# Kernel tuning notes

Hardware: AMD Instinct MI355X
Metric: run time of the kernel (lower is better)

## Reference

```python
import jax, jax.numpy as jnp
import numpy as np


def setup_inputs() -> dict:
    key = jax.random.key(0)
    k1, k2, k3 = jax.random.split(key, 3)
    B, T, J, D = 32, 1024, 128, 256  # D = 2 * input_dim
    ctx_embd = jax.random.normal(k1, (B, T, D), dtype=jnp.float32)
    query_embd = jax.random.normal(k2, (B, J, D), dtype=jnp.float32)
    # nn.Linear(6*input_dim, 1, bias=False) weight flattened: [w1 | w2 | w3], each of size D
    w = jax.random.normal(k3, (3 * D,), dtype=jnp.float32) * (1.0 / np.sqrt(3 * D))
    return {"ctx_embd": ctx_embd, "query_embd": query_embd, "w": w}


def reference(ctx_embd, query_embd, w):
    D = ctx_embd.shape[-1]
    w1, w2, w3 = w[:D], w[D:2 * D], w[2 * D:]
    # Trilinear score S[b,t,j] = ctx.w1 + query.w2 + (ctx*query).w3, decomposed
    # (algebraically identical to Linear(cat(ctx, query, ctx*query))).
    s_ctx = ctx_embd @ w1            # [B, T]
    s_qry = query_embd @ w2          # [B, J]
    s_mul = jnp.einsum('btd,bjd->btj', ctx_embd * w3, query_embd)  # [B, T, J]
    S = s_ctx[:, :, None] + s_qry[:, None, :] + s_mul              # [B, T, J]
    # Context-to-query attention
    a = jax.nn.softmax(S, axis=-1)                                 # [B, T, J]
    c2q = jnp.einsum('btj,bjd->btd', a, query_embd)                # [B, T, D]
    # Query-to-context attention
    b = jax.nn.softmax(jnp.max(S, axis=2), axis=-1)                # [B, T]
    q2c = jnp.einsum('bt,btd->bd', b, ctx_embd)[:, None, :]        # [B, 1, D] broadcast over T
    G = jnp.concatenate(
        [ctx_embd, c2q, ctx_embd * c2q, ctx_embd * q2c], axis=-1)  # [B, T, 4D]
    return G
```

## Files before the change

### kernel.cpp

```cpp
#include <hip/hip_runtime.h>

typedef float f4 __attribute__((ext_vector_type(4)));
typedef float f2 __attribute__((ext_vector_type(2)));
typedef short s8v __attribute__((ext_vector_type(8)));
typedef unsigned int u2v __attribute__((ext_vector_type(2)));
typedef unsigned int u4v __attribute__((ext_vector_type(4)));

#define B_ 32
#define T_ 1024
#define J_ 128
#define D_ 256

__device__ inline unsigned short f2bf(float x) {
    unsigned int u = __float_as_uint(x);
    u += 0x7fffu + ((u >> 16) & 1u);
    return (unsigned short)(u >> 16);
}

__device__ __forceinline__ void ldsload16(const void* g, void* l) {
    __builtin_amdgcn_global_load_lds(
        (const __attribute__((address_space(1))) void*)g,
        (__attribute__((address_space(3))) void*)l, 16, 0, 0);
}

__global__ __launch_bounds__(256) void k_pre(const float* __restrict__ q, const float* __restrict__ w,
                                             unsigned short* __restrict__ Bqh, float* __restrict__ sq,
                                             unsigned short* __restrict__ qTh) {
    __shared__ float t_[16][260];
    int b = blockIdx.x >> 3, jt = blockIdx.x & 7;
    int tid = threadIdx.x;
    const float* qb = q + (b * J_ + jt * 16) * D_;

#pragma unroll
    for (int k = 0; k < 4; k++) {
        int idx = tid + (k << 8);
        int jj = idx >> 6, d4 = idx & 63;
        f4 v = *(const f4*)(qb + jj * D_ + (d4 << 2));
        *(f4*)&t_[jj][d4 << 2] = v;
        f4 w1v = *(const f4*)(w + (d4 << 2));
        f4 w3v = *(const f4*)(w + 2 * D_ + (d4 << 2));
        u2v p;
        p[0] = (unsigned int)f2bf(w3v[0] * v[0] + w1v[0]) | ((unsigned int)f2bf(w3v[1] * v[1] + w1v[1]) << 16);
        p[1] = (unsigned int)f2bf(w3v[2] * v[2] + w1v[2]) | ((unsigned int)f2bf(w3v[3] * v[3] + w1v[3]) << 16);
        *(u2v*)(Bqh + (b * J_ + jt * 16 + jj) * D_ + (d4 << 2)) = p;
    }
    __syncthreads();

    {
        int jj = tid >> 4, dg = tid & 15;
        float p = 0.f;
#pragma unroll
        for (int i = 0; i < 16; i++) {
            int d = (dg << 4) + i;
            p += t_[jj][d] * w[D_ + d];
        }
#pragma unroll
        for (int m = 8; m >= 1; m >>= 1) p += __shfl_xor(p, m);
        if (dg == 0) sq[b * J_ + jt * 16 + jj] = p;
    }

    {
        int dd = tid;
        unsigned int pk[8];
#pragma unroll
        for (int i = 0; i < 8; i++) {
            pk[i] = (unsigned int)f2bf(t_[2 * i][dd]) | ((unsigned int)f2bf(t_[2 * i + 1][dd]) << 16);
        }
        u4v v0, v1;
        v0[0] = pk[0]; v0[1] = pk[1]; v0[2] = pk[2]; v0[3] = pk[3];
        v1[0] = pk[4]; v1[1] = pk[5]; v1[2] = pk[6]; v1[3] = pk[7];
        unsigned short* dst = qTh + (b * D_ + dd) * J_ + jt * 16;
        *(u4v*)dst = v0;
        *(u4v*)(dst + 8) = v1;
    }
}

__global__ __launch_bounds__(256, 4) void k_main(const float* __restrict__ ctx,
                                                 const unsigned short* __restrict__ Bqh,
                                                 const unsigned short* __restrict__ qTh,
                                                 const float* __restrict__ sq,
                                                 float* __restrict__ pq2c, float* __restrict__ pms,
                                                 float* __restrict__ out) {
    __shared__ __align__(16) char lds[40960];
    char* B0 = lds;
    char* B1 = lds + 16384;
    char* Ps = lds + 32768;
    float* sc = (float*)B1;

    int bid = blockIdx.x;
    int b  = ((bid & 7) << 2) | ((bid >> 3) & 3);
    int tc = bid >> 5;
    int t0 = tc << 5;
    int tid = threadIdx.x;
    int w = tid >> 6, l = tid & 63, lr = l & 15, lq = l >> 4;
    int rg = w & 1, ch = w >> 1;
    int R0 = rg << 4;

    const unsigned short* BqB  = Bqh + b * J_ * D_;
    const unsigned short* qThB = qTh + b * D_ * J_;

    auto stageBq = [&](char* buf, int qt) {
#pragma unroll
        for (int i = 0; i < 4; i++) {
            int g = tid + (i << 8);
            int jr = g >> 3, c = g & 7;
            ldsload16(BqB + jr * D_ + (qt << 6) + ((c ^ (jr & 7)) << 3),
                      buf + (i << 12) + (w << 10));
        }
    };
    auto stageQ = [&](char* buf, int st) {
#pragma unroll
        for (int i = 0; i < 4; i++) {
            int g = tid + (i << 8);
            int dr = g >> 4, c = g & 15;
            ldsload16(qThB + ((st << 6) + dr) * J_ + ((c ^ (dr & 7)) << 3),
                      buf + (i << 12) + (w << 10));
        }
    };

    f4 acc[4];
#pragma unroll
    for (int nf = 0; nf < 4; nf++) acc[nf] = (f4){0.f, 0.f, 0.f, 0.f};

    stageBq(B0, 0);
    stageBq(B1, 1);

    const float* ctxA = ctx + (b * T_ + t0 + R0 + lr) * D_;
    s8v af[8];
#pragma unroll
    for (int k = 0; k < 8; k++) {
        f4 a0 = *(const f4*)(ctxA + k * 32 + lq * 8);
        f4 a1 = *(const f4*)(ctxA + k * 32 + lq * 8 + 4);
        union { unsigned short u[8]; s8v v; } t;
#pragma unroll
        for (int e = 0; e < 4; e++) { t.u[e] = f2bf(a0[e]); t.u[e + 4] = f2bf(a1[e]); }
        af[k] = t.v;
    }

    auto mfmaA = [&](char* buf, int qt) {
#pragma unroll
        for (int kk = 0; kk < 2; kk++)
#pragma unroll
            for (int nf = 0; nf < 4; nf++) {
                int jr = (ch << 6) + (nf << 4) + lr;
                s8v bv = *(const s8v*)(buf + (jr << 7) + ((((kk << 2) | lq) ^ (jr & 7)) << 4));
                acc[nf] = __builtin_amdgcn_mfma_f32_16x16x32_bf16(af[(qt << 1) | kk], bv, acc[nf], 0, 0, 0);
            }
    };

    __syncthreads();
    mfmaA(B0, 0);
    __syncthreads();
    stageBq(B0, 2);
    mfmaA(B1, 1);
    __syncthreads();
    stageBq(B1, 3);
    mfmaA(B0, 2);
    __syncthreads();
    stageQ(B0, 0);
    mfmaA(B1, 3);

    float sqv[4];
#pragma unroll
    for (int nf = 0; nf < 4; nf++) sqv[nf] = sq[b * J_ + (ch << 6) + (nf << 4) + lr];
    float mp[4], sp[4];
#pragma unroll
    for (int r = 0; r < 4; r++) {
        float m = -1e30f;
#pragma unroll
        for (int nf = 0; nf < 4; nf++) { acc[nf][r] += sqv[nf]; m = fmaxf(m, acc[nf][r]); }
#pragma unroll
        for (int msk = 8; msk >= 1; msk >>= 1) m = fmaxf(m, __shfl_xor(m, msk));
        float s = 0.f;
#pragma unroll
        for (int nf = 0; nf < 4; nf++) { float e = __expf(acc[nf][r] - m); acc[nf][r] = e; s += e; }
#pragma unroll
        for (int msk = 8; msk >= 1; msk >>= 1) s += __shfl_xor(s, msk);
        mp[r] = m; sp[r] = s;
    }
    __syncthreads();
    if (lr == 0) {
#pragma unroll
        for (int r = 0; r < 4; r++) {
            int row = R0 + (lq << 2) + r;
            sc[(row << 2) + (ch << 1)] = mp[r];
            sc[(row << 2) + (ch << 1) + 1] = sp[r];
        }
    }
    __syncthreads();

    float mm[4];
#pragma unroll
    for (int r = 0; r < 4; r++) {
        int row = R0 + (lq << 2) + r;
        float m0 = sc[(row << 2)],     s0 = sc[(row << 2) + 1];
        float m1 = sc[(row << 2) + 2], s1 = sc[(row << 2) + 3];
        float m = fmaxf(m0, m1);
        float sum = s0 * __expf(m0 - m) + s1 * __expf(m1 - m);
        float scale = __expf(mp[r] - m) / sum;
#pragma unroll
        for (int nf = 0; nf < 4; nf++) {
            int cc = (ch << 6) + (nf << 4) + lr;
            int chunk = cc >> 3;
            *(unsigned short*)(Ps + row * 256 + ((chunk ^ (row & 7)) << 4) + ((lr & 7) << 1)) =
                f2bf(acc[nf][r] * scale);
        }
        mm[r] = m;
    }
    __syncthreads();
    stageQ(B1, 1);

    int prow = R0 + lr;
    s8v pf[4];
#pragma unroll
    for (int jk = 0; jk < 4; jk++)
        pf[jk] = *(const s8v*)(Ps + prow * 256 + ((((jk << 2) + lq) ^ (prow & 7)) << 4));

    f4 acc2[8];
#pragma unroll
    for (int ai = 0; ai < 8; ai++) acc2[ai] = (f4){0.f, 0.f, 0.f, 0.f};

    auto mfmaB = [&](char* rb, int s) {
#pragma unroll
        for (int df2 = 0; df2 < 2; df2++) {
            int dr = (ch << 5) + (df2 << 4) + lr;
            int ai = (s << 1) + df2;
#pragma unroll
            for (int jk = 0; jk < 4; jk++) {
                s8v bv = *(const s8v*)(rb + (dr << 8) + ((((jk << 2) + lq) ^ (dr & 7)) << 4));
                acc2[ai] = __builtin_amdgcn_mfma_f32_16x16x32_bf16(pf[jk], bv, acc2[ai], 0, 0, 0);
            }
        }
    };

    mfmaB(B0, 0);
    __syncthreads();
    stageQ(B0, 2);
    mfmaB(B1, 1);
    __syncthreads();
    stageQ(B1, 3);
    mfmaB(B0, 2);
    __syncthreads();
    mfmaB(B1, 3);
    __syncthreads();

    float* cq = (float*)lds;
#pragma unroll
    for (int s2 = 0; s2 < 4; s2++)
#pragma unroll
        for (int df2 = 0; df2 < 2; df2++) {
            int col = (s2 << 6) + (ch << 5) + (df2 << 4) + lr;
            int ai = (s2 << 1) + df2;
            int chunk = col >> 2;
#pragma unroll
            for (int r = 0; r < 4; r++) {
                int row = R0 + (lq << 2) + r;
                *(float*)((char*)cq + (row << 10) + ((chunk ^ (row & 7)) << 4) + ((col & 3) << 2)) = acc2[ai][r];
            }
        }
    __syncthreads();

    {
        int row = tid >> 3;
        int o = b * T_ + t0 + row;
        const float* crow = ctx + o * D_;
        float* orow = out + o * 1024;
#pragma unroll
        for (int i = 0; i < 8; i++) {
            int col4 = (i << 5) + ((tid & 7) << 2);
            int chunk = col4 >> 2;
            f4 val = *(const f4*)((char*)cq + (row << 10) + ((chunk ^ (row & 7)) << 4));
            f4 cx = *(const f4*)(crow + col4);
            f4 v3 = cx * val;
            __builtin_nontemporal_store(cx, (f4*)(orow + col4));
            __builtin_nontemporal_store(val, (f4*)(orow + 256 + col4));
            __builtin_nontemporal_store(v3, (f4*)(orow + 512 + col4));
        }
    }

    {
        float m16[16];
#pragma unroll
        for (int i = 0; i < 16; i++) m16[i] = __shfl(mm[i & 3], (i >> 2) << 4);
        float mw = -1e30f;
#pragma unroll
        for (int i = 0; i < 16; i++) mw = fmaxf(mw, m16[i]);
        const float* cp = ctx + (b * T_ + t0 + R0) * D_ + (ch << 7) + (l << 1);
        f2 p = (f2){0.f, 0.f};
        float sw_ = 0.f;
#pragma unroll 4
        for (int t = 0; t < 16; t++) {
            float e = __expf(m16[t] - mw);
            sw_ += e;
            f2 cv = *(const f2*)(cp + t * D_);
            p.x += e * cv.x; p.y += e * cv.y;
        }
        int pidx = (((b << 5) | tc) << 1) | rg;
        *(f2*)(pq2c + (pidx << 8) + (ch << 7) + (l << 1)) = p;
        if (ch == 0 && l == 0) { pms[pidx * 2] = mw; pms[pidx * 2 + 1] = sw_; }
    }
}

__global__ __launch_bounds__(256) void k_tail(const float* __restrict__ ctx,
                                              const float* __restrict__ pq2c, const float* __restrict__ pms,
                                              float* __restrict__ out) {
    int b = blockIdx.x >> 5, tc = blockIdx.x & 31;
    int tid = threadIdx.x;
    const float* pm = pms + b * 128;

    float mx = -1e30f;
#pragma unroll 8
    for (int i = 0; i < 64; i++) mx = fmaxf(mx, pm[2 * i]);
    float sm = 0.f, q2 = 0.f;
#pragma unroll 4
    for (int i = 0; i < 64; i++) {
        float e = __expf(pm[2 * i] - mx);
        sm += pm[2 * i + 1] * e;
        q2 += e * pq2c[((b << 6) + i) * 256 + tid];
    }
    q2 /= sm;
    __shared__ float q2s[256];
    q2s[tid] = q2;
    __syncthreads();

    int row = tid >> 3;
    int o = b * T_ + tc * 32 + row;
    const float* crow = ctx + o * D_;
    float* orow = out + o * 1024;
#pragma unroll
    for (int i = 0; i < 8; i++) {
        int col4 = (i << 5) + ((tid & 7) << 2);
        f4 cx = *(const f4*)(crow + col4);
        f4 qv = *(const f4*)&q2s[col4];
        f4 r = cx * qv;
        __builtin_nontemporal_store(r, (f4*)(orow + 768 + col4));
    }
}

extern "C" void kernel_launch(void* const* d_in, const int* in_sizes, int n_in,
                              void* d_out, int out_size, void* d_ws, size_t ws_size,
                              hipStream_t stream) {
    const float* ctx   = (const float*)d_in[0];
    const float* query = (const float*)d_in[1];
    const float* w     = (const float*)d_in[2];
    float* out = (float*)d_out;

    unsigned short* Bqh = (unsigned short*)d_ws;
    unsigned short* qTh = Bqh + B_ * J_ * D_;
    float* fws = (float*)(qTh + B_ * J_ * D_);
    float* sq   = fws;
    float* pq2c = fws + 4096;
    float* pms  = fws + 4096 + 2048 * 256;

    k_pre<<<B_ * 8, 256, 0, stream>>>(query, w, Bqh, sq, qTh);
    k_main<<<B_ * (T_ / 32), 256, 0, stream>>>(ctx, Bqh, qTh, sq, pq2c, pms, out);
    k_tail<<<B_ * 32, 256, 0, stream>>>(ctx, pq2c, pms, out);
}
```

Measured before the change: 66.74 us.

## Process 64 rows per 512-thread block sharing staged query tiles

After: 76.97 us. 1.15x slower.

```diff
diff --git a/kernel.cpp b/kernel.cpp
--- a/kernel.cpp
+++ b/kernel.cpp
@@ -75,46 +75,51 @@
     }
 }
 
-__global__ __launch_bounds__(256, 4) void k_main(const float* __restrict__ ctx,
+__global__ __launch_bounds__(512, 6) void k_main(const float* __restrict__ ctx,
                                                  const unsigned short* __restrict__ Bqh,
                                                  const unsigned short* __restrict__ qTh,
                                                  const float* __restrict__ sq,
                                                  float* __restrict__ pq2c, float* __restrict__ pms,
                                                  float* __restrict__ out) {
-    __shared__ __align__(16) char lds[40960];
+    __shared__ __align__(16) char lds[50176];
     char* B0 = lds;
     char* B1 = lds + 16384;
     char* Ps = lds + 32768;
-    float* sc = (float*)B1;
+    float* sc = (float*)(lds + 49152);
 
     int bid = blockIdx.x;
     int b  = ((bid & 7) << 2) | ((bid >> 3) & 3);
-    int tc = bid >> 5;
-    int t0 = tc << 5;
+    int tt = bid >> 5;
+    int t0 = tt << 6;
     int tid = threadIdx.x;
     int w = tid >> 6, l = tid & 63, lr = l & 15, lq = l >> 4;
-    int rg = w & 1, ch = w >> 1;
+    int pair = w >> 2, wp = w & 3;
+    int rg = wp & 1, ch = wp >> 1;
     int R0 = rg << 4;
+    int tb = t0 + (pair << 5);
+
+    char* Psp = Ps + (pair << 13);
+    float* scp = sc + (pair << 7);
 
     const unsigned short* BqB  = Bqh + b * J_ * D_;
     const unsigned short* qThB = qTh + b * D_ * J_;
 
     auto stageBq = [&](char* buf, int qt) {
 #pragma unroll
-        for (int i = 0; i < 4; i++) {
-            int g = tid + (i << 8);
+        for (int i = 0; i < 2; i++) {
+            int g = tid + (i << 9);
             int jr = g >> 3, c = g & 7;
             ldsload16(BqB + jr * D_ + (qt << 6) + ((c ^ (jr & 7)) << 3),
-                      buf + (i << 12) + (w << 10));
+                      buf + (i << 13) + (w << 10));
         }
     };
     auto stageQ = [&](char* buf, int st) {
 #pragma unroll
-        for (int i = 0; i < 4; i++) {
-            int g = tid + (i << 8);
+        for (int i = 0; i < 2; i++) {
+            int g = tid + (i << 9);
             int dr = g >> 4, c = g & 15;
             ldsload16(qThB + ((st << 6) + dr) * J_ + ((c ^ (dr & 7)) << 3),
-                      buf + (i << 12) + (w << 10));
+                      buf + (i << 13) + (w << 10));
         }
     };
 
@@ -125,7 +130,7 @@
     stageBq(B0, 0);
     stageBq(B1, 1);
 
-    const float* ctxA = ctx + (b * T_ + t0 + R0 + lr) * D_;
+    const float* ctxA = ctx + (b * T_ + tb + R0 + lr) * D_;
     s8v af[8];
 #pragma unroll
     for (int k = 0; k < 8; k++) {
@@ -163,7 +168,7 @@
     float sqv[4];
 #pragma unroll
     for (int nf = 0; nf < 4; nf++) sqv[nf] = sq[b * J_ + (ch << 6) + (nf << 4) + lr];
-    float mp[4], sp[4];
+    float mp[4];
 #pragma unroll
     for (int r = 0; r < 4; r++) {
         float m = -1e30f;
@@ -176,25 +181,22 @@
         for (int nf = 0; nf < 4; nf++) { float e = __expf(acc[nf][r] - m); acc[nf][r] = e; s += e; }
 #pragma unroll
         for (int msk = 8; msk >= 1; msk >>= 1) s += __shfl_xor(s, msk);
-        mp[r] = m; sp[r] = s;
-    }
-    __syncthreads();
-    if (lr == 0) {
-#pragma unroll
-        for (int r = 0; r < 4; r++) {
+        mp[r] = m;
+        if (lr == 0) {
             int row = R0 + (lq << 2) + r;
-            sc[(row << 2) + (ch << 1)] = mp[r];
-            sc[(row << 2) + (ch << 1) + 1] = sp[r];
-        }
-    }
-    __syncthreads();
+            scp[(row << 2) + (ch << 1)] = m;
+            scp[(row << 2) + (ch << 1) + 1] = s;
+        }
+    }
+    __syncthreads();
+    stageQ(B1, 1);
 
     float mm[4];
 #pragma unroll
     for (int r = 0; r < 4; r++) {
         int row = R0 + (lq << 2) + r;
-        float m0 = sc[(row << 2)],     s0 = sc[(row << 2) + 1];
-        float m1 = sc[(row << 2) + 2], s1 = sc[(row << 2) + 3];
+        float m0 = scp[(row << 2)],     s0 = scp[(row << 2) + 1];
+        float m1 = scp[(row << 2) + 2], s1 = scp[(row << 2) + 3];
         float m = fmaxf(m0, m1);
         float sum = s0 * __expf(m0 - m) + s1 * __expf(m1 - m);
         float scale = __expf(mp[r] - m) / sum;
@@ -202,19 +204,18 @@
         for (int nf = 0; nf < 4; nf++) {
             int cc = (ch << 6) + (nf << 4) + lr;
             int chunk = cc >> 3;
-            *(unsigned short*)(Ps + row * 256 + ((chunk ^ (row & 7)) << 4) + ((lr & 7) << 1)) =
+            *(unsigned short*)(Psp + row * 256 + ((chunk ^ (row & 7)) << 4) + ((lr & 7) << 1)) =
                 f2bf(acc[nf][r] * scale);
         }
         mm[r] = m;
     }
     __syncthreads();
-    stageQ(B1, 1);
 
     int prow = R0 + lr;
     s8v pf[4];
 #pragma unroll
     for (int jk = 0; jk < 4; jk++)
-        pf[jk] = *(const s8v*)(Ps + prow * 256 + ((((jk << 2) + lq) ^ (prow & 7)) << 4));
+        pf[jk] = *(const s8v*)(Psp + prow * 256 + ((((jk << 2) + lq) ^ (prow & 7)) << 4));
 
     f4 acc2[8];
 #pragma unroll
@@ -246,36 +247,41 @@
 
     float* cq = (float*)lds;
 #pragma unroll
-    for (int s2 = 0; s2 < 4; s2++)
-#pragma unroll
-        for (int df2 = 0; df2 < 2; df2++) {
-            int col = (s2 << 6) + (ch << 5) + (df2 << 4) + lr;
-            int ai = (s2 << 1) + df2;
-            int chunk = col >> 2;
-#pragma unroll
-            for (int r = 0; r < 4; r++) {
-                int row = R0 + (lq << 2) + r;
-                *(float*)((char*)cq + (row << 10) + ((chunk ^ (row & 7)) << 4) + ((col & 3) << 2)) = acc2[ai][r];
+    for (int p = 0; p < 2; p++) {
+        if (pair == p) {
+#pragma unroll
+            for (int s2 = 0; s2 < 4; s2++)
+#pragma unroll
+                for (int df2 = 0; df2 < 2; df2++) {
+                    int col = (s2 << 6) + (ch << 5) + (df2 << 4) + lr;
+                    int ai = (s2 << 1) + df2;
+                    int chunk = col >> 2;
+#pragma unroll
+                    for (int r = 0; r < 4; r++) {
+                        int row = R0 + (lq << 2) + r;
+                        *(float*)((char*)cq + (row << 10) + ((chunk ^ (row & 7)) << 4) + ((col & 3) << 2)) = acc2[ai][r];
+                    }
+                }
+        }
+        __syncthreads();
+        {
+            int row = tid >> 4;
+            int o = b * T_ + t0 + (p << 5) + row;
+            const float* crow = ctx + o * D_;
+            float* orow = out + o * 1024;
+#pragma unroll
+            for (int i = 0; i < 4; i++) {
+                int col4 = (i << 6) + ((tid & 15) << 2);
+                int chunk = col4 >> 2;
+                f4 val = *(const f4*)((char*)cq + (row << 10) + ((chunk ^ (row & 7)) << 4));
+                f4 cx = *(const f4*)(crow + col4);
+                f4 v3 = cx * val;
+                __builtin_nontemporal_store(cx, (f4*)(orow + col4));
+                __builtin_nontemporal_store(val, (f4*)(orow + 256 + col4));
+                __builtin_nontemporal_store(v3, (f4*)(orow + 512 + col4));
             }
         }
-    __syncthreads();
-
-    {
-        int row = tid >> 3;
-        int o = b * T_ + t0 + row;
-        const float* crow = ctx + o * D_;
-        float* orow = out + o * 1024;
-#pragma unroll
-        for (int i = 0; i < 8; i++) {
-            int col4 = (i << 5) + ((tid & 7) << 2);
-            int chunk = col4 >> 2;
-            f4 val = *(const f4*)((char*)cq + (row << 10) + ((chunk ^ (row & 7)) << 4));
-            f4 cx = *(const f4*)(crow + col4);
-            f4 v3 = cx * val;
-            __builtin_nontemporal_store(cx, (f4*)(orow + col4));
-            __builtin_nontemporal_store(val, (f4*)(orow + 256 + col4));
-            __builtin_nontemporal_store(v3, (f4*)(orow + 512 + col4));
-        }
+        __syncthreads();
     }
 
     {
@@ -285,7 +291,7 @@
         float mw = -1e30f;
 #pragma unroll
         for (int i = 0; i < 16; i++) mw = fmaxf(mw, m16[i]);
-        const float* cp = ctx + (b * T_ + t0 + R0) * D_ + (ch << 7) + (l << 1);
+        const float* cp = ctx + (b * T_ + tb + R0) * D_ + (ch << 7) + (l << 1);
         f2 p = (f2){0.f, 0.f};
         float sw_ = 0.f;
 #pragma unroll 4
@@ -295,7 +301,8 @@
             f2 cv = *(const f2*)(cp + t * D_);
             p.x += e * cv.x; p.y += e * cv.y;
         }
-        int pidx = (((b << 5) | tc) << 1) | rg;
+        int tc32 = (tt << 1) | pair;
+        int pidx = (((b << 5) | tc32) << 1) | rg;
         *(f2*)(pq2c + (pidx << 8) + (ch << 7) + (l << 1)) = p;
         if (ch == 0 && l == 0) { pms[pidx * 2] = mw; pms[pidx * 2 + 1] = sw_; }
     }
@@ -353,6 +360,6 @@
     float* pms  = fws + 4096 + 2048 * 256;
 
     k_pre<<<B_ * 8, 256, 0, stream>>>(query, w, Bqh, sq, qTh);
-    k_main<<<B_ * (T_ / 32), 256, 0, stream>>>(ctx, Bqh, qTh, sq, pq2c, pms, out);
+    k_main<<<B_ * (T_ / 64), 512, 0, stream>>>(ctx, Bqh, qTh, sq, pq2c, pms, out);
     k_tail<<<B_ * 32, 256, 0, stream>>>(ctx, pq2c, pms, out);
 }
```

## Replace syncthreads with counted vmcnt waits to keep next tile loads in flight

Applied to the files above, without the earlier changes.

After: 67.24 us. No clear change (+0.8%).

```diff
diff --git a/kernel.cpp b/kernel.cpp
--- a/kernel.cpp
+++ b/kernel.cpp
@@ -10,6 +10,12 @@
 #define T_ 1024
 #define J_ 128
 #define D_ 256
+
+#define SCHED0 __builtin_amdgcn_sched_barrier(0)
+#define VMWAIT_BAR(N) do { SCHED0; asm volatile("s_waitcnt vmcnt(" #N ")" ::: "memory"); SCHED0; __builtin_amdgcn_s_barrier(); SCHED0; } while (0)
+#define PLAIN_BAR() do { SCHED0; __builtin_amdgcn_s_barrier(); SCHED0; } while (0)
+#define LGKM_BAR() do { SCHED0; asm volatile("s_waitcnt lgkmcnt(0)" ::: "memory"); SCHED0; __builtin_amdgcn_s_barrier(); SCHED0; } while (0)
+#define FULL_BAR() do { SCHED0; asm volatile("s_waitcnt vmcnt(0) lgkmcnt(0)" ::: "memory"); SCHED0; __builtin_amdgcn_s_barrier(); SCHED0; } while (0)
 
 __device__ inline unsigned short f2bf(float x) {
     unsigned int u = __float_as_uint(x);
@@ -118,13 +124,6 @@
         }
     };
 
-    f4 acc[4];
-#pragma unroll
-    for (int nf = 0; nf < 4; nf++) acc[nf] = (f4){0.f, 0.f, 0.f, 0.f};
-
-    stageBq(B0, 0);
-    stageBq(B1, 1);
-
     const float* ctxA = ctx + (b * T_ + t0 + R0 + lr) * D_;
     s8v af[8];
 #pragma unroll
@@ -136,6 +135,15 @@
         for (int e = 0; e < 4; e++) { t.u[e] = f2bf(a0[e]); t.u[e + 4] = f2bf(a1[e]); }
         af[k] = t.v;
     }
+    float sqv[4];
+#pragma unroll
+    for (int nf = 0; nf < 4; nf++) sqv[nf] = sq[b * J_ + (ch << 6) + (nf << 4) + lr];
+    asm volatile("" :: "v"(sqv[0]), "v"(sqv[1]), "v"(sqv[2]), "v"(sqv[3]));
+    SCHED0;
+
+    f4 acc[4];
+#pragma unroll
+    for (int nf = 0; nf < 4; nf++) acc[nf] = (f4){0.f, 0.f, 0.f, 0.f};
 
     auto mfmaA = [&](char* buf, int qt) {
 #pragma unroll
@@ -148,21 +156,23 @@
             }
     };
 
-    __syncthreads();
+    stageBq(B0, 0);
+    stageBq(B1, 1);
+    VMWAIT_BAR(4);
     mfmaA(B0, 0);
-    __syncthreads();
+    PLAIN_BAR();
     stageBq(B0, 2);
+    VMWAIT_BAR(4);
     mfmaA(B1, 1);
-    __syncthreads();
+    PLAIN_BAR();
     stageBq(B1, 3);
+    VMWAIT_BAR(4);
     mfmaA(B0, 2);
-    __syncthreads();
+    PLAIN_BAR();
     stageQ(B0, 0);
+    VMWAIT_BAR(4);
     mfmaA(B1, 3);
 
-    float sqv[4];
-#pragma unroll
-    for (int nf = 0; nf < 4; nf++) sqv[nf] = sq[b * J_ + (ch << 6) + (nf << 4) + lr];
     float mp[4], sp[4];
 #pragma unroll
     for (int r = 0; r < 4; r++) {
@@ -178,7 +188,7 @@
         for (int msk = 8; msk >= 1; msk >>= 1) s += __shfl_xor(s, msk);
         mp[r] = m; sp[r] = s;
     }
-    __syncthreads();
+    PLAIN_BAR();
     if (lr == 0) {
 #pragma unroll
         for (int r = 0; r < 4; r++) {
@@ -187,7 +197,7 @@
             sc[(row << 2) + (ch << 1) + 1] = sp[r];
         }
     }
-    __syncthreads();
+    LGKM_BAR();
 
     float mm[4];
 #pragma unroll
@@ -207,7 +217,8 @@
         }
         mm[r] = m;
     }
-    __syncthreads();
+    FULL_BAR();
+
     stageQ(B1, 1);
 
     int prow = R0 + lr;
@@ -234,13 +245,15 @@
     };
 
     mfmaB(B0, 0);
-    __syncthreads();
+    PLAIN_BAR();
     stageQ(B0, 2);
+    VMWAIT_BAR(4);
     mfmaB(B1, 1);
-    __syncthreads();
+    PLAIN_BAR();
     stageQ(B1, 3);
+    VMWAIT_BAR(4);
     mfmaB(B0, 2);
-    __syncthreads();
+    VMWAIT_BAR(0);
     mfmaB(B1, 3);
     __syncthreads();
 
```
